# Performance work log

Measured on AMD Instinct MI355X. Metric: run time of the kernel, lower is better.

## Reference

```python
import jax, jax.numpy as jnp
import numpy as np

TEMPERATURE = 0.07


def setup_inputs() -> dict:
    B, NB_PER, K, M, D = 32, 128, 8, 4, 256  # batches, bsl1k per batch, dict targets per batch, embeds per target, feat dim
    key = jax.random.key(0)
    kb, kd = jax.random.split(key)
    feats_bsl1k = jax.random.normal(kb, (B * NB_PER, D), dtype=jnp.float32)
    feats_dict = jax.random.normal(kd, (B * K * M, D), dtype=jnp.float32)
    # dict side: per batch, K distinct targets (first one is the mouthing word), M embeddings each
    batch_dict = np.repeat(np.arange(B), K * M).astype(np.int32)
    targets_dict = np.repeat(np.arange(B * K), M).astype(np.int32)  # sorted, distinct across batches
    one_mouth = np.concatenate([np.ones(1, np.int32), np.zeros(K - 1, np.int32)])
    is_mouthing_dict = np.tile(np.repeat(one_mouth, M), B).astype(np.int32)
    # bsl1k side: half the clips carry the batch's mouthing target, half are background (-1)
    batch_bsl1k = np.repeat(np.arange(B), NB_PER).astype(np.int32)
    tb = np.full((B, NB_PER), -1, dtype=np.int32)
    tb[:, : NB_PER // 2] = (np.arange(B, dtype=np.int32) * K)[:, None]
    targets_bsl1k = tb.reshape(-1)
    unique_targets = np.arange(B * K, dtype=np.int32)  # == unique_consecutive(targets_dict)
    return {
        "feats_bsl1k": feats_bsl1k,
        "feats_dict": feats_dict,
        "targets_bsl1k": jnp.asarray(targets_bsl1k),
        "targets_dict": jnp.asarray(targets_dict),
        "batch_bsl1k": jnp.asarray(batch_bsl1k),
        "batch_dict": jnp.asarray(batch_dict),
        "is_mouthing_dict": jnp.asarray(is_mouthing_dict),
        "unique_targets": jnp.asarray(unique_targets),
        "n_batches": B,
    }


def _loss(feats_bsl1k, feats_dict, targets_bsl1k, targets_dict, batch_bsl1k,
          batch_dict, is_mouthing_dict, unique_targets, n_batches):
    G = unique_targets.shape[0]
    fb = feats_bsl1k / jnp.linalg.norm(feats_bsl1k, axis=1, keepdims=True)
    fd = feats_dict / jnp.linalg.norm(feats_dict, axis=1, keepdims=True)
    dist = (fb @ fd.T) / TEMPERATURE  # [Nb, Nd]

    # group index of each dict embedding (unique_targets is sorted)
    g_idx = jnp.searchsorted(unique_targets, targets_dict).astype(jnp.int32)  # [Nd]
    # per-batch mouthing word (exactly one per batch, mirrors .item() in torch)
    mouth_word = jax.ops.segment_max(
        jnp.where(is_mouthing_dict == 1, targets_dict, -1), batch_dict, num_segments=n_batches)
    group_batch = jax.ops.segment_max(batch_dict, g_idx, num_segments=G)
    group_is_mouth = jax.ops.segment_max(is_mouthing_dict, g_idx, num_segments=G)

    # match[i, g]: bsl1k embedding i matches dict target group g (== match_multi collapsed per target)
    is_fg = targets_bsl1k != -1
    mw = mouth_word[batch_bsl1k]  # [Nb]
    match = jnp.where(
        is_fg[:, None],
        unique_targets[None, :] == mw[:, None],
        (group_batch[None, :] == batch_bsl1k[:, None]) & (group_is_mouth[None, :] == 0),
    )  # [Nb, G] bool

    # diff_batch_match: matched pairs from different batches are excluded from the denominator
    DB = match[:, g_idx] & (batch_bsl1k[:, None] != batch_dict[None, :])  # [Nb, Nd]

    c = jax.lax.stop_gradient(jnp.max(dist))  # shared lse shift; cancels in den - num
    E = jnp.exp(dist - c)                     # raw pair weights (numerator)
    A = jnp.where(DB, 0.0, E)                 # denominator weights with cross-batch matches removed
    matchf = match.astype(dist.dtype)

    Ecg = jax.ops.segment_sum(E.T, g_idx, num_segments=G)  # [G, Nb] column-group sums
    Acg = jax.ops.segment_sum(A.T, g_idx, num_segments=G)  # [G, Nb]

    # numerator[g] = lse over cross product {matched bsl1k rows} x {group-g dict cols}
    num_sum = jnp.einsum('gi,ig->g', Ecg, matchf)
    # denominator[g] = lse over union (group cols OR matched rows) minus cross-batch matches,
    # via inclusion-exclusion: cols + rows - intersection
    t1 = jax.ops.segment_sum(A.sum(0), g_idx, num_segments=G)
    t2 = jnp.einsum('ig,i->g', matchf, A.sum(1))
    t3 = jnp.einsum('gi,ig->g', Acg, matchf)
    den_sum = t1 + t2 - t3
    return jnp.mean(jnp.log(den_sum) - jnp.log(num_sum))


def reference(feats_bsl1k, feats_dict, targets_bsl1k, targets_dict, batch_bsl1k,
              batch_dict, is_mouthing_dict, unique_targets, n_batches):
    return _loss(feats_bsl1k, feats_dict, targets_bsl1k, targets_dict, batch_bsl1k,
                 batch_dict, is_mouthing_dict, unique_targets, n_batches)
```

## Files before the change

### kernel.cpp

```cpp
#include <hip/hip_runtime.h>
#include <math.h>

#define INVT (1.0f / 0.07f)
#define CSHIFT (1.0f / 0.07f)

using bf16x8 = __attribute__((ext_vector_type(8))) short;
using f32x4  = __attribute__((ext_vector_type(4))) float;

__device__ __forceinline__ int lower_bound_i(const int* a, int n, int v) {
    int lo = 0, hi = n;
    while (lo < hi) { int mid = (lo + hi) >> 1; if (a[mid] < v) lo = mid + 1; else hi = mid; }
    return lo;
}

__device__ __forceinline__ unsigned short f2bf(float x) {
    unsigned int u = __float_as_uint(x);
    unsigned int r = (u + 0x7fffu + ((u >> 16) & 1u)) >> 16;
    return (unsigned short)r;
}

__device__ __forceinline__ float agent_ld(const float* p) {
    return __hip_atomic_load(p, __ATOMIC_RELAXED, __HIP_MEMORY_SCOPE_AGENT);
}
__device__ __forceinline__ void agent_st(float* p, float v) {
    __hip_atomic_store(p, v, __ATOMIC_RELAXED, __HIP_MEMORY_SCOPE_AGENT);
}

__global__ void k_prep(const float* __restrict__ fb, const float* __restrict__ fd,
                       int Nb, int Nd, int D,
                       unsigned short* __restrict__ fbt, unsigned short* __restrict__ fdt,
                       unsigned int* __restrict__ zbase, int zcount,
                       const int* __restrict__ td, const int* __restrict__ bd,
                       const int* __restrict__ im,
                       int* __restrict__ mouth_word) {
    int zidx = blockIdx.x * blockDim.x + threadIdx.x;
    if (zidx < zcount) zbase[zidx] = 0u;

    int gw = zidx >> 6;
    int lane = threadIdx.x & 63;
    int ktiles = D >> 5;
    if (gw < Nb + Nd) {
        const float* row; unsigned short* ob; int rt, r;
        if (gw < Nb) {
            row = fb + (size_t)gw * D; ob = fbt; rt = gw >> 4; r = gw & 15;
        } else {
            int j = gw - Nb;
            row = fd + (size_t)j * D; ob = fdt; rt = j >> 4; r = j & 15;
        }
        float s = 0.f;
        for (int d = lane * 4; d < D; d += 256) {
            float4 v = *(const float4*)(row + d);
            s += v.x * v.x + v.y * v.y + v.z * v.z + v.w * v.w;
        }
        #pragma unroll
        for (int m = 32; m >= 1; m >>= 1) s += __shfl_xor(s, m, 64);
        float inv = rsqrtf(s);
        for (int d = lane * 4; d < D; d += 256) {
            float4 v = *(const float4*)(row + d);
            ushort4 o;
            o.x = f2bf(v.x * inv); o.y = f2bf(v.y * inv);
            o.z = f2bf(v.z * inv); o.w = f2bf(v.w * inv);
            int kt = d >> 5, kk = d & 31;
            int slot = (kk >> 3) * 16 + r, elem = kk & 7;
            *(ushort4*)(ob + (((size_t)(rt * ktiles + kt)) << 9) + slot * 8 + elem) = o;
        }
    }
    if (blockIdx.x == 0) {
        int t = threadIdx.x;
        for (int i = t; i < Nb; i += blockDim.x) mouth_word[i] = -1;
        __syncthreads();
        for (int j = t; j < Nd; j += blockDim.x) {
            if (im[j] == 1) atomicMax(&mouth_word[bd[j]], td[j]);
        }
    }
}

__global__ __launch_bounds__(256, 4)
void k_main(const unsigned short* __restrict__ fbt, const unsigned short* __restrict__ fdt,
            const int* __restrict__ tb, const int* __restrict__ bb_arr,
            const int* __restrict__ td, const int* __restrict__ bd,
            const int* __restrict__ im, const int* __restrict__ ut,
            const int* __restrict__ mouth_word,
            int Nb, int Nd, int D, int G,
            float* __restrict__ rowpart, float* __restrict__ colpart,
            float* __restrict__ mnum, float* __restrict__ m1, float* __restrict__ m3,
            float* __restrict__ t2g, float* __restrict__ bgs,
            unsigned int* __restrict__ rowcnt, unsigned int* __restrict__ colcnt,
            unsigned int* __restrict__ dcnt, float* __restrict__ out) {
    __shared__ float cnum[64], ct1[64], ct3[64], rsum[64];
    __shared__ int rowflag, colflag, lastflag;

    int t = threadIdx.x, lane = t & 63, wid = t >> 6;
    int wr = wid >> 1, wc = wid & 1;
    int bm = blockIdx.x * 64, bn = blockIdx.y * 64;
    int l15 = lane & 15, lhi = lane >> 4;

    if (t < 64) { cnum[t] = 0.f; ct1[t] = 0.f; ct3[t] = 0.f; rsum[t] = 0.f; }

    int ktiles = D >> 5;
    const unsigned short* a0p = fbt + (((size_t)(((bm >> 4) + wr * 2) * ktiles)) << 9) + lane * 8;
    const unsigned short* a1p = a0p + ((size_t)ktiles << 9);
    const unsigned short* b0p = fdt + (((size_t)(((bn >> 4) + wc * 2) * ktiles)) << 9) + lane * 8;
    const unsigned short* b1p = b0p + ((size_t)ktiles << 9);

    f32x4 acc[2][2] = {};
    bf16x8 ca0 = *(const bf16x8*)a0p;
    bf16x8 ca1 = *(const bf16x8*)a1p;
    bf16x8 cb0 = *(const bf16x8*)b0p;
    bf16x8 cb1 = *(const bf16x8*)b1p;
    size_t o = 0;
    #pragma unroll 7
    for (int kt = 0; kt + 1 < ktiles; ++kt) {
        o += 512;
        bf16x8 na0 = *(const bf16x8*)(a0p + o);
        bf16x8 na1 = *(const bf16x8*)(a1p + o);
        bf16x8 nb0 = *(const bf16x8*)(b0p + o);
        bf16x8 nb1 = *(const bf16x8*)(b1p + o);
        acc[0][0] = __builtin_amdgcn_mfma_f32_16x16x32_bf16(ca0, cb0, acc[0][0], 0, 0, 0);
        acc[0][1] = __builtin_amdgcn_mfma_f32_16x16x32_bf16(ca0, cb1, acc[0][1], 0, 0, 0);
        acc[1][0] = __builtin_amdgcn_mfma_f32_16x16x32_bf16(ca1, cb0, acc[1][0], 0, 0, 0);
        acc[1][1] = __builtin_amdgcn_mfma_f32_16x16x32_bf16(ca1, cb1, acc[1][1], 0, 0, 0);
        ca0 = na0; ca1 = na1; cb0 = nb0; cb1 = nb1;
    }
    acc[0][0] = __builtin_amdgcn_mfma_f32_16x16x32_bf16(ca0, cb0, acc[0][0], 0, 0, 0);
    acc[0][1] = __builtin_amdgcn_mfma_f32_16x16x32_bf16(ca0, cb1, acc[0][1], 0, 0, 0);
    acc[1][0] = __builtin_amdgcn_mfma_f32_16x16x32_bf16(ca1, cb0, acc[1][0], 0, 0, 0);
    acc[1][1] = __builtin_amdgcn_mfma_f32_16x16x32_bf16(ca1, cb1, acc[1][1], 0, 0, 0);

    int cgb[2], cgm[2], cgc[2];
    #pragma unroll
    for (int nj = 0; nj < 2; ++nj) {
        int col = bn + wc * 32 + nj * 16 + l15;
        cgb[nj] = bd[col]; cgm[nj] = im[col]; cgc[nj] = td[col];
    }

    float pnum[2] = {0.f, 0.f}, pt1[2] = {0.f, 0.f}, pt3[2] = {0.f, 0.f};
    float prow[2][4];

    #pragma unroll
    for (int mi = 0; mi < 2; ++mi) {
        #pragma unroll
        for (int r = 0; r < 4; ++r) {
            int i = bm + wr * 32 + mi * 16 + lhi * 4 + r;
            int tbi = tb[i], bbi = bb_arr[i];
            int mw = mouth_word[bbi];
            bool fg = (tbi != -1);
            float pr = 0.f;
            #pragma unroll
            for (int nj = 0; nj < 2; ++nj) {
                float e = __expf(acc[mi][nj][r] * INVT - CSHIFT);
                bool match = fg ? (cgc[nj] == mw) : ((cgb[nj] == bbi) && (cgm[nj] == 0));
                float a = (match && (bbi != cgb[nj])) ? 0.f : e;
                pnum[nj] += match ? e : 0.f;
                pt1[nj] += a;
                pt3[nj] += match ? a : 0.f;
                pr += a;
            }
            prow[mi][r] = pr;
        }
    }

    __syncthreads();

    #pragma unroll
    for (int nj = 0; nj < 2; ++nj) {
        float n = pnum[nj], x1 = pt1[nj], x3 = pt3[nj];
        n  += __shfl_xor(n, 16, 64);  n  += __shfl_xor(n, 32, 64);
        x1 += __shfl_xor(x1, 16, 64); x1 += __shfl_xor(x1, 32, 64);
        x3 += __shfl_xor(x3, 16, 64); x3 += __shfl_xor(x3, 32, 64);
        if (lhi == 0) {
            int c = wc * 32 + nj * 16 + l15;
            atomicAdd(&cnum[c], n); atomicAdd(&ct1[c], x1); atomicAdd(&ct3[c], x3);
        }
    }
    #pragma unroll
    for (int mi = 0; mi < 2; ++mi) {
        #pragma unroll
        for (int r = 0; r < 4; ++r) {
            float v = prow[mi][r];
            v += __shfl_xor(v, 1, 64); v += __shfl_xor(v, 2, 64);
            v += __shfl_xor(v, 4, 64); v += __shfl_xor(v, 8, 64);
            if (l15 == 0) atomicAdd(&rsum[wr * 32 + mi * 16 + lhi * 4 + r], v);
        }
    }
    __syncthreads();

    float* cp = colpart + (size_t)(blockIdx.x & 7) * 3 * Nd;
    if (t < 64) {
        atomicAdd(&cp[bn + t], cnum[t]);
        atomicAdd(&cp[Nd + bn + t], ct1[t]);
        atomicAdd(&cp[2 * Nd + bn + t], ct3[t]);
    } else if (t < 128) {
        atomicAdd(&rowpart[(size_t)(blockIdx.y & 3) * Nb + bm + (t - 64)], rsum[t - 64]);
    }

    asm volatile("s_waitcnt vmcnt(0)" ::: "memory");
    __syncthreads();
    if (t == 0) {
        rowflag = (atomicAdd(&rowcnt[blockIdx.x * 16], 1u) == gridDim.y - 1) ? 1 : 0;
        colflag = (atomicAdd(&colcnt[blockIdx.y * 16], 1u) == gridDim.x - 1) ? 1 : 0;
    }
    __syncthreads();
    int nfin = rowflag + colflag;
    if (nfin == 0) return;

    if (rowflag && t < 64) {
        int i = bm + t;
        float r = agent_ld(&rowpart[i]) + agent_ld(&rowpart[Nb + i])
                + agent_ld(&rowpart[2 * Nb + i]) + agent_ld(&rowpart[3 * Nb + i]);
        int tbi = tb[i], bbi = bb_arr[i] & 1023;
        if (tbi != -1) {
            int g = lower_bound_i(ut, G, mouth_word[bbi]);
            atomicAdd(&t2g[g], r);
        } else {
            atomicAdd(&bgs[bbi], r);
        }
    }
    if (colflag && t < 192) {
        int c = t / 3, arr = t - c * 3;
        int col = bn + c;
        float s0 = 0.f;
        #pragma unroll
        for (int p = 0; p < 8; ++p)
            s0 += agent_ld(&colpart[(size_t)p * 3 * Nd + (size_t)arr * Nd + col]);
        float* dst = (arr == 0 ? mnum : (arr == 1 ? m1 : m3)) + col;
        agent_st(dst, s0);
    }

    asm volatile("s_waitcnt vmcnt(0)" ::: "memory");
    __syncthreads();
    if (t == 0) {
        unsigned int newv = atomicAdd(dcnt, (unsigned int)nfin) + (unsigned int)nfin;
        lastflag = (newv == gridDim.x + gridDim.y) ? 1 : 0;
    }
    __syncthreads();
    if (!lastflag) return;

    __shared__ float red[256];
    float acc2 = 0.f;
    for (int g = t; g < G; g += 256) {
        int s = lower_bound_i(td, Nd, ut[g]);
        int e = (g + 1 < G) ? lower_bound_i(td, Nd, ut[g + 1]) : Nd;
        float sn = 0.f, s1 = 0.f, s3 = 0.f;
        for (int c = s; c < e; ++c) {
            sn += agent_ld(&mnum[c]);
            s1 += agent_ld(&m1[c]);
            s3 += agent_ld(&m3[c]);
        }
        int gb = bd[s], gm = im[s];
        float t2 = agent_ld(&t2g[g]);
        if (gm == 0 && gb >= 0 && gb < 1024) t2 += agent_ld(&bgs[gb]);
        acc2 += logf(s1 + t2 - s3) - logf(sn);
    }
    red[t] = acc2;
    __syncthreads();
    for (int k = 128; k >= 1; k >>= 1) {
        if (t < k) red[t] += red[t + k];
        __syncthreads();
    }
    if (t == 0) out[0] = red[0] / (float)G;
}

extern "C" void kernel_launch(void* const* d_in, const int* in_sizes, int n_in,
                              void* d_out, int out_size, void* d_ws, size_t ws_size,
                              hipStream_t stream) {
    const float* fb = (const float*)d_in[0];
    const float* fd = (const float*)d_in[1];
    const int* tb = (const int*)d_in[2];
    const int* td = (const int*)d_in[3];
    const int* bb = (const int*)d_in[4];
    const int* bd = (const int*)d_in[5];
    const int* im = (const int*)d_in[6];
    const int* ut = (const int*)d_in[7];

    int Nb = in_sizes[2];
    int Nd = in_sizes[3];
    int G  = in_sizes[7];
    int D  = in_sizes[0] / Nb;
    float* out = (float*)d_out;

    char* p = (char*)d_ws;
    unsigned short* fbt = (unsigned short*)p; p += (size_t)Nb * D * sizeof(unsigned short);
    unsigned short* fdt = (unsigned short*)p; p += (size_t)Nd * D * sizeof(unsigned short);
    char* zstart = p;
    float* rowpart = (float*)p;  p += (size_t)4 * Nb * sizeof(float);
    float* colpart = (float*)p;  p += (size_t)24 * Nd * sizeof(float);
    float* t2g = (float*)p;      p += 1024 * sizeof(float);
    float* bgs = (float*)p;      p += 1024 * sizeof(float);
    unsigned int* rowcnt = (unsigned int*)p; p += 64 * 16 * sizeof(unsigned int);
    unsigned int* colcnt = (unsigned int*)p; p += 16 * 16 * sizeof(unsigned int);
    unsigned int* dcnt = (unsigned int*)p;   p += 16 * sizeof(unsigned int);
    int zcount = (int)((p - zstart) / 4);
    float* mnum = (float*)p; p += (size_t)Nd * sizeof(float);
    float* m1 = (float*)p;   p += (size_t)Nd * sizeof(float);
    float* m3 = (float*)p;   p += (size_t)Nd * sizeof(float);
    int* mouth_word = (int*)p; p += (size_t)Nb * sizeof(int);

    {
        int waves = Nb + Nd;
        int blocks = (waves + 3) / 4;
        k_prep<<<blocks, 256, 0, stream>>>(fb, fd, Nb, Nd, D, fbt, fdt,
                                           (unsigned int*)zstart, zcount,
                                           td, bd, im, mouth_word);
    }

    dim3 grid(Nb / 64, Nd / 64);
    k_main<<<grid, 256, 0, stream>>>(fbt, fdt, tb, bb, td, bd, im, ut, mouth_word,
                                     Nb, Nd, D, G,
                                     rowpart, colpart, mnum, m1, m3, t2g, bgs,
                                     rowcnt, colcnt, dcnt, out);
}
```

Measured before the change: 44.94 us.

## Fuse normalization and bf16 conversion into main kernel, replace atomics with slabs

Removes the separate prep kernel. Each block now loads fp32 rows directly, normalizes them in registers and converts them to bf16 MFMA fragments, and computes the mouthing word per block in shared memory. Partial sums are written with plain stores into per-block slabs instead of atomics, and zeroing moves to hipMemsetAsync. In exchange, every block redundantly reads fp32 inputs (twice the bytes of bf16) and recomputes the norms and the mouth-word scan. The register footprint is also larger, so launch bounds drop to 2.

```diff
diff --git a/kernel.cpp b/kernel.cpp
--- a/kernel.cpp
+++ b/kernel.cpp
@@ -26,68 +26,48 @@
     __hip_atomic_store(p, v, __ATOMIC_RELAXED, __HIP_MEMORY_SCOPE_AGENT);
 }
 
-__global__ void k_prep(const float* __restrict__ fb, const float* __restrict__ fd,
-                       int Nb, int Nd, int D,
-                       unsigned short* __restrict__ fbt, unsigned short* __restrict__ fdt,
-                       unsigned int* __restrict__ zbase, int zcount,
-                       const int* __restrict__ td, const int* __restrict__ bd,
-                       const int* __restrict__ im,
-                       int* __restrict__ mouth_word) {
-    int zidx = blockIdx.x * blockDim.x + threadIdx.x;
-    if (zidx < zcount) zbase[zidx] = 0u;
-
-    int gw = zidx >> 6;
-    int lane = threadIdx.x & 63;
-    int ktiles = D >> 5;
-    if (gw < Nb + Nd) {
-        const float* row; unsigned short* ob; int rt, r;
-        if (gw < Nb) {
-            row = fb + (size_t)gw * D; ob = fbt; rt = gw >> 4; r = gw & 15;
-        } else {
-            int j = gw - Nb;
-            row = fd + (size_t)j * D; ob = fdt; rt = j >> 4; r = j & 15;
-        }
-        float s = 0.f;
-        for (int d = lane * 4; d < D; d += 256) {
-            float4 v = *(const float4*)(row + d);
-            s += v.x * v.x + v.y * v.y + v.z * v.z + v.w * v.w;
-        }
-        #pragma unroll
-        for (int m = 32; m >= 1; m >>= 1) s += __shfl_xor(s, m, 64);
-        float inv = rsqrtf(s);
-        for (int d = lane * 4; d < D; d += 256) {
-            float4 v = *(const float4*)(row + d);
-            ushort4 o;
-            o.x = f2bf(v.x * inv); o.y = f2bf(v.y * inv);
-            o.z = f2bf(v.z * inv); o.w = f2bf(v.w * inv);
-            int kt = d >> 5, kk = d & 31;
-            int slot = (kk >> 3) * 16 + r, elem = kk & 7;
-            *(ushort4*)(ob + (((size_t)(rt * ktiles + kt)) << 9) + slot * 8 + elem) = o;
-        }
-    }
-    if (blockIdx.x == 0) {
-        int t = threadIdx.x;
-        for (int i = t; i < Nb; i += blockDim.x) mouth_word[i] = -1;
-        __syncthreads();
-        for (int j = t; j < Nd; j += blockDim.x) {
-            if (im[j] == 1) atomicMax(&mouth_word[bd[j]], td[j]);
-        }
-    }
-}
-
-__global__ __launch_bounds__(256, 4)
-void k_main(const unsigned short* __restrict__ fbt, const unsigned short* __restrict__ fdt,
-            const int* __restrict__ tb, const int* __restrict__ bb_arr,
-            const int* __restrict__ td, const int* __restrict__ bd,
-            const int* __restrict__ im, const int* __restrict__ ut,
-            const int* __restrict__ mouth_word,
-            int Nb, int Nd, int D, int G,
-            float* __restrict__ rowpart, float* __restrict__ colpart,
-            float* __restrict__ mnum, float* __restrict__ m1, float* __restrict__ m3,
-            float* __restrict__ t2g, float* __restrict__ bgs,
-            unsigned int* __restrict__ rowcnt, unsigned int* __restrict__ colcnt,
-            unsigned int* __restrict__ dcnt, float* __restrict__ out) {
+__device__ __forceinline__ void load_norm_set(const float* p, bf16x8* fr) {
+    float4 v0[8], v1[8];
+    float ss = 0.f;
+    #pragma unroll
+    for (int kt = 0; kt < 8; ++kt) {
+        v0[kt] = *(const float4*)(p + kt * 32);
+        v1[kt] = *(const float4*)(p + kt * 32 + 4);
+        ss += v0[kt].x * v0[kt].x + v0[kt].y * v0[kt].y + v0[kt].z * v0[kt].z + v0[kt].w * v0[kt].w
+            + v1[kt].x * v1[kt].x + v1[kt].y * v1[kt].y + v1[kt].z * v1[kt].z + v1[kt].w * v1[kt].w;
+    }
+    ss += __shfl_xor(ss, 16, 64);
+    ss += __shfl_xor(ss, 32, 64);
+    float inv = rsqrtf(ss);
+    #pragma unroll
+    for (int kt = 0; kt < 8; ++kt) {
+        bf16x8 f;
+        f[0] = (short)f2bf(v0[kt].x * inv);
+        f[1] = (short)f2bf(v0[kt].y * inv);
+        f[2] = (short)f2bf(v0[kt].z * inv);
+        f[3] = (short)f2bf(v0[kt].w * inv);
+        f[4] = (short)f2bf(v1[kt].x * inv);
+        f[5] = (short)f2bf(v1[kt].y * inv);
+        f[6] = (short)f2bf(v1[kt].z * inv);
+        f[7] = (short)f2bf(v1[kt].w * inv);
+        fr[kt] = f;
+    }
+}
+
+__global__ __launch_bounds__(256, 2)
+void k_all(const float* __restrict__ fb, const float* __restrict__ fd,
+           const int* __restrict__ tb, const int* __restrict__ bb_arr,
+           const int* __restrict__ td, const int* __restrict__ bd,
+           const int* __restrict__ im, const int* __restrict__ ut,
+           int Nb, int Nd, int D, int G,
+           float* __restrict__ rowslab, float* __restrict__ colslab,
+           float* __restrict__ mnum, float* __restrict__ m1, float* __restrict__ m3,
+           float* __restrict__ t2g, float* __restrict__ bgs,
+           unsigned int* __restrict__ rowcnt, unsigned int* __restrict__ colcnt,
+           unsigned int* __restrict__ dcnt, float* __restrict__ out) {
     __shared__ float cnum[64], ct1[64], ct3[64], rsum[64];
+    __shared__ int mwl[1024];
+    __shared__ float red[256];
     __shared__ int rowflag, colflag, lastflag;
 
     int t = threadIdx.x, lane = t & 63, wid = t >> 6;
@@ -96,36 +76,31 @@
     int l15 = lane & 15, lhi = lane >> 4;
 
     if (t < 64) { cnum[t] = 0.f; ct1[t] = 0.f; ct3[t] = 0.f; rsum[t] = 0.f; }
-
-    int ktiles = D >> 5;
-    const unsigned short* a0p = fbt + (((size_t)(((bm >> 4) + wr * 2) * ktiles)) << 9) + lane * 8;
-    const unsigned short* a1p = a0p + ((size_t)ktiles << 9);
-    const unsigned short* b0p = fdt + (((size_t)(((bn >> 4) + wc * 2) * ktiles)) << 9) + lane * 8;
-    const unsigned short* b1p = b0p + ((size_t)ktiles << 9);
+    for (int i = t; i < 1024; i += 256) mwl[i] = -1;
+    __syncthreads();
+    for (int j = t; j < Nd; j += 256) {
+        if (im[j] == 1) atomicMax(&mwl[bd[j] & 1023], td[j]);
+    }
+
+    const float* pa0 = fb + (size_t)(bm + wr * 32 + l15) * D + lhi * 8;
+    const float* pa1 = pa0 + (size_t)16 * D;
+    const float* pb0 = fd + (size_t)(bn + wc * 32 + l15) * D + lhi * 8;
+    const float* pb1 = pb0 + (size_t)16 * D;
+
+    bf16x8 fa0[8], fa1[8], fb0[8], fb1[8];
+    load_norm_set(pa0, fa0);
+    load_norm_set(pa1, fa1);
+    load_norm_set(pb0, fb0);
+    load_norm_set(pb1, fb1);
 
     f32x4 acc[2][2] = {};
-    bf16x8 ca0 = *(const bf16x8*)a0p;
-    bf16x8 ca1 = *(const bf16x8*)a1p;
-    bf16x8 cb0 = *(const bf16x8*)b0p;
-    bf16x8 cb1 = *(const bf16x8*)b1p;
-    size_t o = 0;
-    #pragma unroll 7
-    for (int kt = 0; kt + 1 < ktiles; ++kt) {
-        o += 512;
-        bf16x8 na0 = *(const bf16x8*)(a0p + o);
-        bf16x8 na1 = *(const bf16x8*)(a1p + o);
-        bf16x8 nb0 = *(const bf16x8*)(b0p + o);
-        bf16x8 nb1 = *(const bf16x8*)(b1p + o);
-        acc[0][0] = __builtin_amdgcn_mfma_f32_16x16x32_bf16(ca0, cb0, acc[0][0], 0, 0, 0);
-        acc[0][1] = __builtin_amdgcn_mfma_f32_16x16x32_bf16(ca0, cb1, acc[0][1], 0, 0, 0);
-        acc[1][0] = __builtin_amdgcn_mfma_f32_16x16x32_bf16(ca1, cb0, acc[1][0], 0, 0, 0);
-        acc[1][1] = __builtin_amdgcn_mfma_f32_16x16x32_bf16(ca1, cb1, acc[1][1], 0, 0, 0);
-        ca0 = na0; ca1 = na1; cb0 = nb0; cb1 = nb1;
-    }
-    acc[0][0] = __builtin_amdgcn_mfma_f32_16x16x32_bf16(ca0, cb0, acc[0][0], 0, 0, 0);
-    acc[0][1] = __builtin_amdgcn_mfma_f32_16x16x32_bf16(ca0, cb1, acc[0][1], 0, 0, 0);
-    acc[1][0] = __builtin_amdgcn_mfma_f32_16x16x32_bf16(ca1, cb0, acc[1][0], 0, 0, 0);
-    acc[1][1] = __builtin_amdgcn_mfma_f32_16x16x32_bf16(ca1, cb1, acc[1][1], 0, 0, 0);
+    #pragma unroll
+    for (int kt = 0; kt < 8; ++kt) {
+        acc[0][0] = __builtin_amdgcn_mfma_f32_16x16x32_bf16(fa0[kt], fb0[kt], acc[0][0], 0, 0, 0);
+        acc[0][1] = __builtin_amdgcn_mfma_f32_16x16x32_bf16(fa0[kt], fb1[kt], acc[0][1], 0, 0, 0);
+        acc[1][0] = __builtin_amdgcn_mfma_f32_16x16x32_bf16(fa1[kt], fb0[kt], acc[1][0], 0, 0, 0);
+        acc[1][1] = __builtin_amdgcn_mfma_f32_16x16x32_bf16(fa1[kt], fb1[kt], acc[1][1], 0, 0, 0);
+    }
 
     int cgb[2], cgm[2], cgc[2];
     #pragma unroll
@@ -143,7 +118,7 @@
         for (int r = 0; r < 4; ++r) {
             int i = bm + wr * 32 + mi * 16 + lhi * 4 + r;
             int tbi = tb[i], bbi = bb_arr[i];
-            int mw = mouth_word[bbi];
+            int mw = mwl[bbi & 1023];
             bool fg = (tbi != -1);
             float pr = 0.f;
             #pragma unroll
@@ -185,13 +160,12 @@
     }
     __syncthreads();
 
-    float* cp = colpart + (size_t)(blockIdx.x & 7) * 3 * Nd;
     if (t < 64) {
-        atomicAdd(&cp[bn + t], cnum[t]);
-        atomicAdd(&cp[Nd + bn + t], ct1[t]);
-        atomicAdd(&cp[2 * Nd + bn + t], ct3[t]);
-    } else if (t < 128) {
-        atomicAdd(&rowpart[(size_t)(blockIdx.y & 3) * Nb + bm + (t - 64)], rsum[t - 64]);
+        agent_st(&rowslab[(size_t)blockIdx.y * Nb + bm + t], rsum[t]);
+    } else {
+        int c = (t - 64) & 63, arr = (t - 64) >> 6;
+        float v = (arr == 0) ? cnum[c] : (arr == 1 ? ct1[c] : ct3[c]);
+        agent_st(&colslab[((size_t)blockIdx.x * 3 + arr) * Nd + bn + c], v);
     }
 
     asm volatile("s_waitcnt vmcnt(0)" ::: "memory");
@@ -206,11 +180,11 @@
 
     if (rowflag && t < 64) {
         int i = bm + t;
-        float r = agent_ld(&rowpart[i]) + agent_ld(&rowpart[Nb + i])
-                + agent_ld(&rowpart[2 * Nb + i]) + agent_ld(&rowpart[3 * Nb + i]);
+        float r = 0.f;
+        for (int q = 0; q < (int)gridDim.y; ++q) r += agent_ld(&rowslab[(size_t)q * Nb + i]);
         int tbi = tb[i], bbi = bb_arr[i] & 1023;
         if (tbi != -1) {
-            int g = lower_bound_i(ut, G, mouth_word[bbi]);
+            int g = lower_bound_i(ut, G, mwl[bbi]);
             atomicAdd(&t2g[g], r);
         } else {
             atomicAdd(&bgs[bbi], r);
@@ -220,9 +194,8 @@
         int c = t / 3, arr = t - c * 3;
         int col = bn + c;
         float s0 = 0.f;
-        #pragma unroll
-        for (int p = 0; p < 8; ++p)
-            s0 += agent_ld(&colpart[(size_t)p * 3 * Nd + (size_t)arr * Nd + col]);
+        for (int x = 0; x < (int)gridDim.x; ++x)
+            s0 += agent_ld(&colslab[((size_t)x * 3 + arr) * Nd + col]);
         float* dst = (arr == 0 ? mnum : (arr == 1 ? m1 : m3)) + col;
         agent_st(dst, s0);
     }
@@ -236,7 +209,6 @@
     __syncthreads();
     if (!lastflag) return;
 
-    __shared__ float red[256];
     float acc2 = 0.f;
     for (int g = t; g < G; g += 256) {
         int s = lower_bound_i(td, Nd, ut[g]);
@@ -279,34 +251,27 @@
     int D  = in_sizes[0] / Nb;
     float* out = (float*)d_out;
 
+    int gx = Nb / 64, gy = Nd / 64;
+
     char* p = (char*)d_ws;
-    unsigned short* fbt = (unsigned short*)p; p += (size_t)Nb * D * sizeof(unsigned short);
-    unsigned short* fdt = (unsigned short*)p; p += (size_t)Nd * D * sizeof(unsigned short);
-    char* zstart = p;
-    float* rowpart = (float*)p;  p += (size_t)4 * Nb * sizeof(float);
-    float* colpart = (float*)p;  p += (size_t)24 * Nd * sizeof(float);
-    float* t2g = (float*)p;      p += 1024 * sizeof(float);
-    float* bgs = (float*)p;      p += 1024 * sizeof(float);
-    unsigned int* rowcnt = (unsigned int*)p; p += 64 * 16 * sizeof(unsigned int);
-    unsigned int* colcnt = (unsigned int*)p; p += 16 * 16 * sizeof(unsigned int);
-    unsigned int* dcnt = (unsigned int*)p;   p += 16 * sizeof(unsigned int);
-    int zcount = (int)((p - zstart) / 4);
+    float* rowslab = (float*)p; p += (size_t)gy * Nb * sizeof(float);
+    float* colslab = (float*)p; p += (size_t)gx * 3 * Nd * sizeof(float);
     float* mnum = (float*)p; p += (size_t)Nd * sizeof(float);
     float* m1 = (float*)p;   p += (size_t)Nd * sizeof(float);
     float* m3 = (float*)p;   p += (size_t)Nd * sizeof(float);
-    int* mouth_word = (int*)p; p += (size_t)Nb * sizeof(int);
-
-    {
-        int waves = Nb + Nd;
-        int blocks = (waves + 3) / 4;
-        k_prep<<<blocks, 256, 0, stream>>>(fb, fd, Nb, Nd, D, fbt, fdt,
-                                           (unsigned int*)zstart, zcount,
-                                           td, bd, im, mouth_word);
-    }
-
-    dim3 grid(Nb / 64, Nd / 64);
-    k_main<<<grid, 256, 0, stream>>>(fbt, fdt, tb, bb, td, bd, im, ut, mouth_word,
-                                     Nb, Nd, D, G,
-                                     rowpart, colpart, mnum, m1, m3, t2g, bgs,
-                                     rowcnt, colcnt, dcnt, out);
-}
+    char* zstart = p;
+    float* t2g = (float*)p;  p += 1024 * sizeof(float);
+    float* bgs = (float*)p;  p += 1024 * sizeof(float);
+    unsigned int* rowcnt = (unsigned int*)p; p += (size_t)gx * 16 * sizeof(unsigned int);
+    unsigned int* colcnt = (unsigned int*)p; p += (size_t)gy * 16 * sizeof(unsigned int);
+    unsigned int* dcnt = (unsigned int*)p;   p += 16 * sizeof(unsigned int);
+    size_t zbytes = (size_t)(p - zstart);
+
+    hipMemsetAsync(zstart, 0, zbytes, stream);
+
+    dim3 grid(gx, gy);
+    k_all<<<grid, 256, 0, stream>>>(fb, fd, tb, bb, td, bd, im, ut,
+                                    Nb, Nd, D, G,
+                                    rowslab, colslab, mnum, m1, m3, t2g, bgs,
+                                    rowcnt, colcnt, dcnt, out);
+}
```

New measurement: 106.4 us. 2.37x slower.
